# Performance work log

Measured on AMD Instinct MI355X. Metric: run time of the kernel, lower is better.

## Reference

```python
import jax, jax.numpy as jnp
import numpy as np

N_HEADS = 16
D_MODEL = 1024
D_HEAD = D_MODEL // N_HEADS  # 64


def setup_inputs() -> dict:
    key = jax.random.key(0)
    ks = jax.random.split(key, 7)
    B, S = 16, 1024
    x = jax.random.normal(ks[0], (B, S, D_MODEL), dtype=jnp.float32)
    # Per-head torch Linear params: weight [out, in] = [D_HEAD, D_HEAD], bias [D_HEAD].
    # Xavier-uniform scale for square weight: sqrt(6/(fan_in+fan_out)).
    lim = float(np.sqrt(6.0 / (D_HEAD + D_HEAD)))
    blim = float(1.0 / np.sqrt(D_HEAD))  # torch default bias init U(-1/sqrt(fan_in), ...)
    Wq = jax.random.uniform(ks[1], (N_HEADS, D_HEAD, D_HEAD), jnp.float32, -lim, lim)
    Wk = jax.random.uniform(ks[2], (N_HEADS, D_HEAD, D_HEAD), jnp.float32, -lim, lim)
    Wv = jax.random.uniform(ks[3], (N_HEADS, D_HEAD, D_HEAD), jnp.float32, -lim, lim)
    bq = jax.random.uniform(ks[4], (N_HEADS, D_HEAD), jnp.float32, -blim, blim)
    bk = jax.random.uniform(ks[5], (N_HEADS, D_HEAD), jnp.float32, -blim, blim)
    bv = jax.random.uniform(ks[6], (N_HEADS, D_HEAD), jnp.float32, -blim, blim)
    return {"sequences": x, "Wq": Wq, "Wk": Wk, "Wv": Wv, "bq": bq, "bk": bk, "bv": bv}


def reference(sequences, Wq, Wk, Wv, bq, bk, bv):
    B, S, D = sequences.shape
    H, dh = N_HEADS, D_HEAD
    # Split feature dim into heads: [B, S, H, dh] (same chunks the torch loop slices).
    x = sequences.reshape(B, S, H, dh)
    # torch Linear: y = x @ W.T + b  -> einsum over the 'in' axis of W[out, in].
    q = jnp.einsum("bshd,hed->bshe", x, Wq) + bq  # [B,S,H,dh]
    k = jnp.einsum("bshd,hed->bshe", x, Wk) + bk
    v = jnp.einsum("bshd,hed->bshe", x, Wv) + bv
    scale = 1.0 / jnp.sqrt(jnp.asarray(dh, dtype=sequences.dtype))
    scores = jnp.einsum("bshe,bthe->bhst", q, k) * scale  # [B,H,S,S]
    weights = jax.nn.softmax(scores, axis=-1)
    attended = jnp.einsum("bhst,bthe->bshe", weights, v)  # [B,S,H,dh]
    # hstack over heads == concat along feature dim.
    return attended.reshape(B, S, D)
```

## Files before the change

### kernel.cpp

```cpp
#include <hip/hip_runtime.h>

constexpr int B_ = 16, S_ = 1024, H_ = 16, DH_ = 64, DM_ = 1024;

typedef short bf16x8 __attribute__((ext_vector_type(8)));
typedef unsigned short us8 __attribute__((ext_vector_type(8)));
typedef unsigned short us4 __attribute__((ext_vector_type(4)));
typedef float f32x4 __attribute__((ext_vector_type(4)));
typedef float f32x16 __attribute__((ext_vector_type(16)));
typedef unsigned u32x4 __attribute__((ext_vector_type(4)));

__device__ __forceinline__ unsigned short f2b(float f) {
    unsigned u = __builtin_bit_cast(unsigned, f);
    u += 0x7FFFu + ((u >> 16) & 1u);
    return (unsigned short)(u >> 16);
}

__device__ __forceinline__ int swz(int r, int c) { return (r << 6) + (c ^ ((r & 7) << 3)); }

__device__ __forceinline__ unsigned cvtpk(float lo, float hi) {
    unsigned r;
    asm("v_cvt_pk_bf16_f32 %0, %1, %2" : "=v"(r) : "v"(lo), "v"(hi));
    return r;
}
__device__ __forceinline__ void permswap(unsigned& a, unsigned& b) {
    asm volatile("v_permlane32_swap_b32 %0, %1" : "+v"(a), "+v"(b));
}

__device__ __forceinline__ void gload16(const unsigned short* g, unsigned short* l) {
    __builtin_amdgcn_global_load_lds(
        (const __attribute__((address_space(1))) void*)g,
        (__attribute__((address_space(3))) void*)l, 16, 0, 0);
}

#define BAR_VM(N) do { \
    asm volatile("s_waitcnt vmcnt(" #N ") lgkmcnt(0)" ::: "memory"); \
    __builtin_amdgcn_sched_barrier(0); \
    __builtin_amdgcn_s_barrier(); \
    __builtin_amdgcn_sched_barrier(0); \
} while (0)

#define QSCALE 0.18033688011112042f

__global__ __launch_bounds__(256) void proj_kernel(
    const float* __restrict__ x,
    const float* __restrict__ wq, const float* __restrict__ wk, const float* __restrict__ wv,
    const float* __restrict__ bq, const float* __restrict__ bk, const float* __restrict__ bv,
    unsigned short* __restrict__ qo, unsigned short* __restrict__ ko,
    unsigned short* __restrict__ vto)
{
    __shared__ unsigned short xs[128 * 64];
    __shared__ unsigned short wls[3][64 * 64];

    const int tid = threadIdx.x;
    const int bid = blockIdx.x;
    const int chunk = bid & 7, bh = bid >> 3;
    const int b = bh >> 4, h = bh & 15;
    const int s0 = chunk * 128;
    const int lane = tid & 63, w = tid >> 6;
    const int lr = lane & 15, lg = lane >> 4;

    #pragma unroll
    for (int it = 0; it < 4; ++it) {
        int item = it * 256 + tid;
        int row = item >> 3, c = (item & 7) << 3;
        const float* src = x + (size_t)(b * S_ + s0 + row) * DM_ + h * DH_ + c;
        float4 f0 = *(const float4*)src;
        float4 f1 = *(const float4*)(src + 4);
        us8 v = { f2b(f0.x), f2b(f0.y), f2b(f0.z), f2b(f0.w),
                  f2b(f1.x), f2b(f1.y), f2b(f1.z), f2b(f1.w) };
        *(us8*)&xs[swz(row, c)] = v;
    }
    const float* wsrc[3] = { wq, wk, wv };
    #pragma unroll
    for (int mtx = 0; mtx < 3; ++mtx) {
        const float scl = (mtx == 0) ? QSCALE : 1.0f;
        #pragma unroll
        for (int it = 0; it < 2; ++it) {
            int item = it * 256 + tid;
            int row = item >> 3, c = (item & 7) << 3;
            const float* src = wsrc[mtx] + (size_t)h * 4096 + row * 64 + c;
            float4 f0 = *(const float4*)src;
            float4 f1 = *(const float4*)(src + 4);
            us8 v = { f2b(f0.x * scl), f2b(f0.y * scl), f2b(f0.z * scl), f2b(f0.w * scl),
                      f2b(f1.x * scl), f2b(f1.y * scl), f2b(f1.z * scl), f2b(f1.w * scl) };
            *(us8*)&wls[mtx][swz(row, c)] = v;
        }
    }
    __syncthreads();

    bf16x8 af[2][2];
    #pragma unroll
    for (int mt = 0; mt < 2; ++mt)
        #pragma unroll
        for (int k2 = 0; k2 < 2; ++k2)
            af[mt][k2] = *(const bf16x8*)&xs[swz(w * 32 + mt * 16 + lr, k2 * 32 + lg * 8)];

    const float* bias[3] = { bq, bk, bv };
    #pragma unroll
    for (int mtx = 0; mtx < 3; ++mtx) {
        const float bscl = (mtx == 0) ? QSCALE : 1.0f;
        #pragma unroll
        for (int mt = 0; mt < 2; ++mt) {
            #pragma unroll
            for (int n4 = 0; n4 < 4; ++n4) {
                f32x4 acc = { 0.f, 0.f, 0.f, 0.f };
                #pragma unroll
                for (int k2 = 0; k2 < 2; ++k2) {
                    bf16x8 bf_ = *(const bf16x8*)&wls[mtx][swz(n4 * 16 + lr, k2 * 32 + lg * 8)];
                    acc = __builtin_amdgcn_mfma_f32_16x16x32_bf16(af[mt][k2], bf_, acc, 0, 0, 0);
                }
                const int e = n4 * 16 + lr;
                const float bb = bias[mtx][h * DH_ + e] * bscl;
                const int srow0 = s0 + w * 32 + mt * 16 + lg * 4;
                if (mtx == 0) {
                    #pragma unroll
                    for (int r = 0; r < 4; ++r)
                        qo[(size_t)(bh * S_ + srow0 + r) * 64 + e] = f2b(acc[r] + bb);
                } else if (mtx == 1) {
                    #pragma unroll
                    for (int r = 0; r < 4; ++r)
                        ko[(size_t)(bh * S_ + srow0 + r) * 64 + e] = f2b(acc[r] + bb);
                } else {
                    us4 pk = { f2b(acc[0] + bb), f2b(acc[1] + bb),
                               f2b(acc[2] + bb), f2b(acc[3] + bb) };
                    *(us4*)&vto[(size_t)(bh * 64 + e) * S_ + srow0] = pk;
                }
            }
        }
    }
}

__device__ __forceinline__ void qk_tile(const unsigned short* K, const bf16x8 (&qf)[4],
                                        const f32x16& zro, f32x16& p0, f32x16& p1,
                                        int l31, int hi8)
{
    __builtin_amdgcn_s_setprio(1);
    {
        bf16x8 ka0 = *(const bf16x8*)&K[swz(l31,      hi8)];
        bf16x8 ka1 = *(const bf16x8*)&K[swz(32 + l31, hi8)];
        p0 = __builtin_amdgcn_mfma_f32_32x32x16_bf16(ka0, qf[0], zro, 0, 0, 0);
        p1 = __builtin_amdgcn_mfma_f32_32x32x16_bf16(ka1, qf[0], zro, 0, 0, 0);
    }
    #pragma unroll
    for (int s = 1; s < 4; ++s) {
        bf16x8 ka0 = *(const bf16x8*)&K[swz(l31,      s * 16 + hi8)];
        bf16x8 ka1 = *(const bf16x8*)&K[swz(32 + l31, s * 16 + hi8)];
        p0 = __builtin_amdgcn_mfma_f32_32x32x16_bf16(ka0, qf[s], p0, 0, 0, 0);
        p1 = __builtin_amdgcn_mfma_f32_32x32x16_bf16(ka1, qf[s], p1, 0, 0, 0);
    }
    __builtin_amdgcn_s_setprio(0);
}

__device__ __forceinline__ void pv_tile(f32x16& p0, f32x16& p1, const unsigned short* V,
                                        const bf16x8& ones, f32x16& o0, f32x16& o1,
                                        f32x16& lsum, int l31, int hi8)
{
    #pragma unroll
    for (int i = 0; i < 16; ++i) {
        p0[i] = __builtin_amdgcn_exp2f(p0[i]);
        p1[i] = __builtin_amdgcn_exp2f(p1[i]);
    }
    bf16x8 pa[4];
    {
        unsigned a0 = cvtpk(p0[0], p0[1]),  b0 = cvtpk(p0[4], p0[5]);
        unsigned a1 = cvtpk(p0[2], p0[3]),  b1 = cvtpk(p0[6], p0[7]);
        permswap(a0, b0); permswap(a1, b1);
        u32x4 t0 = { a0, a1, b0, b1 };
        pa[0] = __builtin_bit_cast(bf16x8, t0);
        unsigned a2 = cvtpk(p0[8], p0[9]),   b2 = cvtpk(p0[12], p0[13]);
        unsigned a3 = cvtpk(p0[10], p0[11]), b3 = cvtpk(p0[14], p0[15]);
        permswap(a2, b2); permswap(a3, b3);
        u32x4 t1 = { a2, a3, b2, b3 };
        pa[1] = __builtin_bit_cast(bf16x8, t1);
        unsigned a4 = cvtpk(p1[0], p1[1]),  b4 = cvtpk(p1[4], p1[5]);
        unsigned a5 = cvtpk(p1[2], p1[3]),  b5 = cvtpk(p1[6], p1[7]);
        permswap(a4, b4); permswap(a5, b5);
        u32x4 t2 = { a4, a5, b4, b5 };
        pa[2] = __builtin_bit_cast(bf16x8, t2);
        unsigned a6 = cvtpk(p1[8], p1[9]),   b6 = cvtpk(p1[12], p1[13]);
        unsigned a7 = cvtpk(p1[10], p1[11]), b7 = cvtpk(p1[14], p1[15]);
        permswap(a6, b6); permswap(a7, b7);
        u32x4 t3 = { a6, a7, b6, b7 };
        pa[3] = __builtin_bit_cast(bf16x8, t3);
    }
    __builtin_amdgcn_s_setprio(1);
    #pragma unroll
    for (int s = 0; s < 4; ++s) {
        bf16x8 vb0 = *(const bf16x8*)&V[swz(l31,      s * 16 + hi8)];
        bf16x8 vb1 = *(const bf16x8*)&V[swz(32 + l31, s * 16 + hi8)];
        o0 = __builtin_amdgcn_mfma_f32_32x32x16_bf16(pa[s], vb0, o0, 0, 0, 0);
        o1 = __builtin_amdgcn_mfma_f32_32x32x16_bf16(pa[s], vb1, o1, 0, 0, 0);
        lsum = __builtin_amdgcn_mfma_f32_32x32x16_bf16(pa[s], ones, lsum, 0, 0, 0);
    }
    __builtin_amdgcn_s_setprio(0);
}

__global__ __launch_bounds__(256) void attn_kernel(
    const unsigned short* __restrict__ qw, const unsigned short* __restrict__ kw,
    const unsigned short* __restrict__ vtw, float* __restrict__ out)
{
    __shared__ unsigned short ks[4][64 * 64];
    __shared__ unsigned short vs[4][64 * 64];

    const int tid = threadIdx.x, lane = tid & 63, w = tid >> 6;
    int bid = blockIdx.x;
    bid = (bid & 7) * 256 + (bid >> 3);
    const int qt = bid & 7, bh = bid >> 3;
    const int b = bh >> 4, h = bh & 15;
    const int q0 = qt * 128;
    const int l31 = lane & 31, hi = lane >> 5, hi8 = hi << 3;

    const unsigned short* kbase = kw + (size_t)bh * S_ * 64;
    const unsigned short* vbase = vtw + (size_t)bh * 64 * S_;

    const int srow8 = lane >> 3;
    const int colsw = ((lane & 7) ^ (lane >> 3)) << 3;

    auto stage = [&](int t) {
        const int bf = t & 3;
        const int n1 = t * 64;
        #pragma unroll
        for (int i = 0; i < 2; ++i) {
            const int br = i * 32 + (w << 3);
            gload16(kbase + (size_t)(n1 + br + srow8) * 64 + colsw, &ks[bf][br * 64]);
            gload16(vbase + (size_t)(br + srow8) * S_ + n1 + colsw, &vs[bf][br * 64]);
        }
    };

    bf16x8 qf[4];
    {
        const unsigned short* qp = qw + (size_t)(bh * S_ + q0 + w * 32 + l31) * 64 + hi8;
        #pragma unroll
        for (int s = 0; s < 4; ++s) qf[s] = *(const bf16x8*)(qp + s * 16);
    }

    const short ONE = (short)0x3F80;
    const bf16x8 ones = { ONE, ONE, ONE, ONE, ONE, ONE, ONE, ONE };

    f32x16 o0, o1, lsum, zro;
    #pragma unroll
    for (int i = 0; i < 16; ++i) { o0[i] = 0.f; o1[i] = 0.f; lsum[i] = 0.f; zro[i] = 0.f; }

    stage(0);
    stage(1);
    stage(2);
    BAR_VM(8);

    f32x16 pA0, pA1, pB0, pB1;
    qk_tile(&ks[0][0], qf, zro, pA0, pA1, l31, hi8);

    constexpr int NT = S_ / 64;
    #pragma unroll 1
    for (int tt = 0; tt < 7; ++tt) {
        const int t0 = 2 * tt;
        BAR_VM(4);
        stage(t0 + 3);
        qk_tile(&ks[(t0 + 1) & 3][0], qf, zro, pB0, pB1, l31, hi8);
        pv_tile(pA0, pA1, &vs[t0 & 3][0], ones, o0, o1, lsum, l31, hi8);
        BAR_VM(4);
        if (t0 + 4 < NT) stage(t0 + 4);
        qk_tile(&ks[(t0 + 2) & 3][0], qf, zro, pA0, pA1, l31, hi8);
        pv_tile(pB0, pB1, &vs[(t0 + 1) & 3][0], ones, o0, o1, lsum, l31, hi8);
    }
    BAR_VM(0);
    qk_tile(&ks[15 & 3][0], qf, zro, pB0, pB1, l31, hi8);
    pv_tile(pA0, pA1, &vs[14 & 3][0], ones, o0, o1, lsum, l31, hi8);
    pv_tile(pB0, pB1, &vs[15 & 3][0], ones, o0, o1, lsum, l31, hi8);

    #pragma unroll
    for (int r = 0; r < 16; ++r) {
        const int q = (r & 3) + 8 * (r >> 2) + (hi << 2);
        const float iv = 1.0f / lsum[r];
        float* op = out + (size_t)(b * S_ + q0 + w * 32 + q) * DM_ + h * DH_ + l31;
        op[0]  = o0[r] * iv;
        op[32] = o1[r] * iv;
    }
}

extern "C" void kernel_launch(void* const* d_in, const int* in_sizes, int n_in,
                              void* d_out, int out_size, void* d_ws, size_t ws_size,
                              hipStream_t stream) {
    const float* x  = (const float*)d_in[0];
    const float* wq = (const float*)d_in[1];
    const float* wk = (const float*)d_in[2];
    const float* wv = (const float*)d_in[3];
    const float* bq = (const float*)d_in[4];
    const float* bk = (const float*)d_in[5];
    const float* bv = (const float*)d_in[6];
    float* out = (float*)d_out;

    const size_t per = (size_t)B_ * H_ * S_ * DH_;
    unsigned short* qws  = (unsigned short*)d_ws;
    unsigned short* kws  = qws + per;
    unsigned short* vtws = kws + per;

    proj_kernel<<<dim3(2048), dim3(256), 0, stream>>>(x, wq, wk, wv, bq, bk, bv,
                                                      qws, kws, vtws);
    attn_kernel<<<dim3(2048), dim3(256), 0, stream>>>(qws, kws, vtws, out);
}
```

Measured before the change: 129.4 us.

## Process two 32-row query tiles per wave to reuse K/V LDS reads

Each wave now handles 64 query rows as two 32-row sub-tiles that share every K and V fragment loaded from LDS. This halves the block count and the total K/V traffic per query. The software-pipelined QK/PV interleave across tiles is replaced by a simple per-tile loop, so the overlap between the QK MFMAs of one tile and the exp/PV of the previous one is lost. Register pressure goes up, and with half as many blocks the GPU may be less well occupied.

```diff
diff --git a/kernel.cpp b/kernel.cpp
--- a/kernel.cpp
+++ b/kernel.cpp
@@ -130,69 +130,28 @@
     }
 }
 
-__device__ __forceinline__ void qk_tile(const unsigned short* K, const bf16x8 (&qf)[4],
-                                        const f32x16& zro, f32x16& p0, f32x16& p1,
-                                        int l31, int hi8)
+__device__ __forceinline__ void cvt_half(const f32x16& p0, const f32x16& p1, bf16x8 (&pa)[4])
 {
-    __builtin_amdgcn_s_setprio(1);
-    {
-        bf16x8 ka0 = *(const bf16x8*)&K[swz(l31,      hi8)];
-        bf16x8 ka1 = *(const bf16x8*)&K[swz(32 + l31, hi8)];
-        p0 = __builtin_amdgcn_mfma_f32_32x32x16_bf16(ka0, qf[0], zro, 0, 0, 0);
-        p1 = __builtin_amdgcn_mfma_f32_32x32x16_bf16(ka1, qf[0], zro, 0, 0, 0);
-    }
-    #pragma unroll
-    for (int s = 1; s < 4; ++s) {
-        bf16x8 ka0 = *(const bf16x8*)&K[swz(l31,      s * 16 + hi8)];
-        bf16x8 ka1 = *(const bf16x8*)&K[swz(32 + l31, s * 16 + hi8)];
-        p0 = __builtin_amdgcn_mfma_f32_32x32x16_bf16(ka0, qf[s], p0, 0, 0, 0);
-        p1 = __builtin_amdgcn_mfma_f32_32x32x16_bf16(ka1, qf[s], p1, 0, 0, 0);
-    }
-    __builtin_amdgcn_s_setprio(0);
-}
-
-__device__ __forceinline__ void pv_tile(f32x16& p0, f32x16& p1, const unsigned short* V,
-                                        const bf16x8& ones, f32x16& o0, f32x16& o1,
-                                        f32x16& lsum, int l31, int hi8)
-{
-    #pragma unroll
-    for (int i = 0; i < 16; ++i) {
-        p0[i] = __builtin_amdgcn_exp2f(p0[i]);
-        p1[i] = __builtin_amdgcn_exp2f(p1[i]);
-    }
-    bf16x8 pa[4];
-    {
-        unsigned a0 = cvtpk(p0[0], p0[1]),  b0 = cvtpk(p0[4], p0[5]);
-        unsigned a1 = cvtpk(p0[2], p0[3]),  b1 = cvtpk(p0[6], p0[7]);
-        permswap(a0, b0); permswap(a1, b1);
-        u32x4 t0 = { a0, a1, b0, b1 };
-        pa[0] = __builtin_bit_cast(bf16x8, t0);
-        unsigned a2 = cvtpk(p0[8], p0[9]),   b2 = cvtpk(p0[12], p0[13]);
-        unsigned a3 = cvtpk(p0[10], p0[11]), b3 = cvtpk(p0[14], p0[15]);
-        permswap(a2, b2); permswap(a3, b3);
-        u32x4 t1 = { a2, a3, b2, b3 };
-        pa[1] = __builtin_bit_cast(bf16x8, t1);
-        unsigned a4 = cvtpk(p1[0], p1[1]),  b4 = cvtpk(p1[4], p1[5]);
-        unsigned a5 = cvtpk(p1[2], p1[3]),  b5 = cvtpk(p1[6], p1[7]);
-        permswap(a4, b4); permswap(a5, b5);
-        u32x4 t2 = { a4, a5, b4, b5 };
-        pa[2] = __builtin_bit_cast(bf16x8, t2);
-        unsigned a6 = cvtpk(p1[8], p1[9]),   b6 = cvtpk(p1[12], p1[13]);
-        unsigned a7 = cvtpk(p1[10], p1[11]), b7 = cvtpk(p1[14], p1[15]);
-        permswap(a6, b6); permswap(a7, b7);
-        u32x4 t3 = { a6, a7, b6, b7 };
-        pa[3] = __builtin_bit_cast(bf16x8, t3);
-    }
-    __builtin_amdgcn_s_setprio(1);
-    #pragma unroll
-    for (int s = 0; s < 4; ++s) {
-        bf16x8 vb0 = *(const bf16x8*)&V[swz(l31,      s * 16 + hi8)];
-        bf16x8 vb1 = *(const bf16x8*)&V[swz(32 + l31, s * 16 + hi8)];
-        o0 = __builtin_amdgcn_mfma_f32_32x32x16_bf16(pa[s], vb0, o0, 0, 0, 0);
-        o1 = __builtin_amdgcn_mfma_f32_32x32x16_bf16(pa[s], vb1, o1, 0, 0, 0);
-        lsum = __builtin_amdgcn_mfma_f32_32x32x16_bf16(pa[s], ones, lsum, 0, 0, 0);
-    }
-    __builtin_amdgcn_s_setprio(0);
+    unsigned a0 = cvtpk(p0[0], p0[1]),  b0 = cvtpk(p0[4], p0[5]);
+    unsigned a1 = cvtpk(p0[2], p0[3]),  b1 = cvtpk(p0[6], p0[7]);
+    permswap(a0, b0); permswap(a1, b1);
+    u32x4 t0 = { a0, a1, b0, b1 };
+    pa[0] = __builtin_bit_cast(bf16x8, t0);
+    unsigned a2 = cvtpk(p0[8], p0[9]),   b2 = cvtpk(p0[12], p0[13]);
+    unsigned a3 = cvtpk(p0[10], p0[11]), b3 = cvtpk(p0[14], p0[15]);
+    permswap(a2, b2); permswap(a3, b3);
+    u32x4 t1 = { a2, a3, b2, b3 };
+    pa[1] = __builtin_bit_cast(bf16x8, t1);
+    unsigned a4 = cvtpk(p1[0], p1[1]),  b4 = cvtpk(p1[4], p1[5]);
+    unsigned a5 = cvtpk(p1[2], p1[3]),  b5 = cvtpk(p1[6], p1[7]);
+    permswap(a4, b4); permswap(a5, b5);
+    u32x4 t2 = { a4, a5, b4, b5 };
+    pa[2] = __builtin_bit_cast(bf16x8, t2);
+    unsigned a6 = cvtpk(p1[8], p1[9]),   b6 = cvtpk(p1[12], p1[13]);
+    unsigned a7 = cvtpk(p1[10], p1[11]), b7 = cvtpk(p1[14], p1[15]);
+    permswap(a6, b6); permswap(a7, b7);
+    u32x4 t3 = { a6, a7, b6, b7 };
+    pa[3] = __builtin_bit_cast(bf16x8, t3);
 }
 
 __global__ __launch_bounds__(256) void attn_kernel(
@@ -204,10 +163,10 @@
 
     const int tid = threadIdx.x, lane = tid & 63, w = tid >> 6;
     int bid = blockIdx.x;
-    bid = (bid & 7) * 256 + (bid >> 3);
-    const int qt = bid & 7, bh = bid >> 3;
+    bid = (bid & 7) * 128 + (bid >> 3);
+    const int qt = bid & 3, bh = bid >> 2;
     const int b = bh >> 4, h = bh & 15;
-    const int q0 = qt * 128;
+    const int q0w = qt * 256 + w * 64;
     const int l31 = lane & 31, hi = lane >> 5, hi8 = hi << 3;
 
     const unsigned short* kbase = kw + (size_t)bh * S_ * 64;
@@ -227,53 +186,102 @@
         }
     };
 
-    bf16x8 qf[4];
+    bf16x8 qfA[4], qfB[4];
     {
-        const unsigned short* qp = qw + (size_t)(bh * S_ + q0 + w * 32 + l31) * 64 + hi8;
-        #pragma unroll
-        for (int s = 0; s < 4; ++s) qf[s] = *(const bf16x8*)(qp + s * 16);
+        const unsigned short* qpA = qw + (size_t)(bh * S_ + q0w + l31) * 64 + hi8;
+        const unsigned short* qpB = qw + (size_t)(bh * S_ + q0w + 32 + l31) * 64 + hi8;
+        #pragma unroll
+        for (int s = 0; s < 4; ++s) {
+            qfA[s] = *(const bf16x8*)(qpA + s * 16);
+            qfB[s] = *(const bf16x8*)(qpB + s * 16);
+        }
     }
 
     const short ONE = (short)0x3F80;
     const bf16x8 ones = { ONE, ONE, ONE, ONE, ONE, ONE, ONE, ONE };
 
-    f32x16 o0, o1, lsum, zro;
-    #pragma unroll
-    for (int i = 0; i < 16; ++i) { o0[i] = 0.f; o1[i] = 0.f; lsum[i] = 0.f; zro[i] = 0.f; }
+    f32x16 oA0, oA1, oB0, oB1, lsumA, lsumB, zro;
+    #pragma unroll
+    for (int i = 0; i < 16; ++i) {
+        oA0[i] = 0.f; oA1[i] = 0.f; oB0[i] = 0.f; oB1[i] = 0.f;
+        lsumA[i] = 0.f; lsumB[i] = 0.f; zro[i] = 0.f;
+    }
 
     stage(0);
     stage(1);
     stage(2);
-    BAR_VM(8);
-
-    f32x16 pA0, pA1, pB0, pB1;
-    qk_tile(&ks[0][0], qf, zro, pA0, pA1, l31, hi8);
 
     constexpr int NT = S_ / 64;
     #pragma unroll 1
-    for (int tt = 0; tt < 7; ++tt) {
-        const int t0 = 2 * tt;
-        BAR_VM(4);
-        stage(t0 + 3);
-        qk_tile(&ks[(t0 + 1) & 3][0], qf, zro, pB0, pB1, l31, hi8);
-        pv_tile(pA0, pA1, &vs[t0 & 3][0], ones, o0, o1, lsum, l31, hi8);
-        BAR_VM(4);
-        if (t0 + 4 < NT) stage(t0 + 4);
-        qk_tile(&ks[(t0 + 2) & 3][0], qf, zro, pA0, pA1, l31, hi8);
-        pv_tile(pB0, pB1, &vs[(t0 + 1) & 3][0], ones, o0, o1, lsum, l31, hi8);
-    }
-    BAR_VM(0);
-    qk_tile(&ks[15 & 3][0], qf, zro, pB0, pB1, l31, hi8);
-    pv_tile(pA0, pA1, &vs[14 & 3][0], ones, o0, o1, lsum, l31, hi8);
-    pv_tile(pB0, pB1, &vs[15 & 3][0], ones, o0, o1, lsum, l31, hi8);
+    for (int t = 0; t < NT; ++t) {
+        if (t < 14)       { BAR_VM(8); }
+        else if (t == 14) { BAR_VM(4); }
+        else              { BAR_VM(0); }
+        if (t + 3 < NT) stage(t + 3);
+
+        const int buf = t & 3;
+        const unsigned short* K = &ks[buf][0];
+        const unsigned short* V = &vs[buf][0];
+
+        f32x16 pA0, pA1, pB0, pB1;
+        __builtin_amdgcn_s_setprio(1);
+        {
+            bf16x8 ka0 = *(const bf16x8*)&K[swz(l31,      hi8)];
+            bf16x8 ka1 = *(const bf16x8*)&K[swz(32 + l31, hi8)];
+            pA0 = __builtin_amdgcn_mfma_f32_32x32x16_bf16(ka0, qfA[0], zro, 0, 0, 0);
+            pA1 = __builtin_amdgcn_mfma_f32_32x32x16_bf16(ka1, qfA[0], zro, 0, 0, 0);
+            pB0 = __builtin_amdgcn_mfma_f32_32x32x16_bf16(ka0, qfB[0], zro, 0, 0, 0);
+            pB1 = __builtin_amdgcn_mfma_f32_32x32x16_bf16(ka1, qfB[0], zro, 0, 0, 0);
+        }
+        #pragma unroll
+        for (int s = 1; s < 4; ++s) {
+            bf16x8 ka0 = *(const bf16x8*)&K[swz(l31,      s * 16 + hi8)];
+            bf16x8 ka1 = *(const bf16x8*)&K[swz(32 + l31, s * 16 + hi8)];
+            pA0 = __builtin_amdgcn_mfma_f32_32x32x16_bf16(ka0, qfA[s], pA0, 0, 0, 0);
+            pA1 = __builtin_amdgcn_mfma_f32_32x32x16_bf16(ka1, qfA[s], pA1, 0, 0, 0);
+            pB0 = __builtin_amdgcn_mfma_f32_32x32x16_bf16(ka0, qfB[s], pB0, 0, 0, 0);
+            pB1 = __builtin_amdgcn_mfma_f32_32x32x16_bf16(ka1, qfB[s], pB1, 0, 0, 0);
+        }
+        __builtin_amdgcn_s_setprio(0);
+
+        #pragma unroll
+        for (int i = 0; i < 16; ++i) {
+            pA0[i] = __builtin_amdgcn_exp2f(pA0[i]);
+            pA1[i] = __builtin_amdgcn_exp2f(pA1[i]);
+            pB0[i] = __builtin_amdgcn_exp2f(pB0[i]);
+            pB1[i] = __builtin_amdgcn_exp2f(pB1[i]);
+        }
+
+        bf16x8 paA[4], paB[4];
+        cvt_half(pA0, pA1, paA);
+        cvt_half(pB0, pB1, paB);
+
+        __builtin_amdgcn_s_setprio(1);
+        #pragma unroll
+        for (int s = 0; s < 4; ++s) {
+            bf16x8 vb0 = *(const bf16x8*)&V[swz(l31,      s * 16 + hi8)];
+            bf16x8 vb1 = *(const bf16x8*)&V[swz(32 + l31, s * 16 + hi8)];
+            oA0 = __builtin_amdgcn_mfma_f32_32x32x16_bf16(paA[s], vb0, oA0, 0, 0, 0);
+            oA1 = __builtin_amdgcn_mfma_f32_32x32x16_bf16(paA[s], vb1, oA1, 0, 0, 0);
+            oB0 = __builtin_amdgcn_mfma_f32_32x32x16_bf16(paB[s], vb0, oB0, 0, 0, 0);
+            oB1 = __builtin_amdgcn_mfma_f32_32x32x16_bf16(paB[s], vb1, oB1, 0, 0, 0);
+            lsumA = __builtin_amdgcn_mfma_f32_32x32x16_bf16(paA[s], ones, lsumA, 0, 0, 0);
+            lsumB = __builtin_amdgcn_mfma_f32_32x32x16_bf16(paB[s], ones, lsumB, 0, 0, 0);
+        }
+        __builtin_amdgcn_s_setprio(0);
+    }
 
     #pragma unroll
     for (int r = 0; r < 16; ++r) {
         const int q = (r & 3) + 8 * (r >> 2) + (hi << 2);
-        const float iv = 1.0f / lsum[r];
-        float* op = out + (size_t)(b * S_ + q0 + w * 32 + q) * DM_ + h * DH_ + l31;
-        op[0]  = o0[r] * iv;
-        op[32] = o1[r] * iv;
+        const float ivA = 1.0f / lsumA[r];
+        const float ivB = 1.0f / lsumB[r];
+        float* opA = out + (size_t)(b * S_ + q0w + q) * DM_ + h * DH_ + l31;
+        float* opB = out + (size_t)(b * S_ + q0w + 32 + q) * DM_ + h * DH_ + l31;
+        opA[0]  = oA0[r] * ivA;
+        opA[32] = oA1[r] * ivA;
+        opB[0]  = oB0[r] * ivB;
+        opB[32] = oB1[r] * ivB;
     }
 }
 
@@ -296,5 +304,5 @@
 
     proj_kernel<<<dim3(2048), dim3(256), 0, stream>>>(x, wq, wk, wv, bq, bk, bv,
                                                       qws, kws, vtws);
-    attn_kernel<<<dim3(2048), dim3(256), 0, stream>>>(qws, kws, vtws, out);
-}
+    attn_kernel<<<dim3(1024), dim3(256), 0, stream>>>(qws, kws, vtws, out);
+}
```

Measured after the change: 167.9 us. +29.7%, slower.

## Drop ones-MFMA row sum, use triple buffering and target three blocks per CU

Applied to the files above, without the earlier changes.

Removes the software-pipelined two-tile QK/PV interleave and replaces it with a simple per-tile loop over a 3-deep LDS ring buffer instead of 4-deep. The row sum previously computed by an extra MFMA against a ones vector is now a VALU reduction plus a cross-half shuffle, and the normalizer is broadcast with a shuffle at the end. Launch bounds request 3 blocks per CU, cutting register and LDS use to raise occupancy. The cost is losing the explicit overlap of QK MFMAs with exp/convert work and adding VALU adds to each tile.

```diff
diff --git a/kernel.cpp b/kernel.cpp
--- a/kernel.cpp
+++ b/kernel.cpp
@@ -130,77 +130,12 @@
     }
 }
 
-__device__ __forceinline__ void qk_tile(const unsigned short* K, const bf16x8 (&qf)[4],
-                                        const f32x16& zro, f32x16& p0, f32x16& p1,
-                                        int l31, int hi8)
-{
-    __builtin_amdgcn_s_setprio(1);
-    {
-        bf16x8 ka0 = *(const bf16x8*)&K[swz(l31,      hi8)];
-        bf16x8 ka1 = *(const bf16x8*)&K[swz(32 + l31, hi8)];
-        p0 = __builtin_amdgcn_mfma_f32_32x32x16_bf16(ka0, qf[0], zro, 0, 0, 0);
-        p1 = __builtin_amdgcn_mfma_f32_32x32x16_bf16(ka1, qf[0], zro, 0, 0, 0);
-    }
-    #pragma unroll
-    for (int s = 1; s < 4; ++s) {
-        bf16x8 ka0 = *(const bf16x8*)&K[swz(l31,      s * 16 + hi8)];
-        bf16x8 ka1 = *(const bf16x8*)&K[swz(32 + l31, s * 16 + hi8)];
-        p0 = __builtin_amdgcn_mfma_f32_32x32x16_bf16(ka0, qf[s], p0, 0, 0, 0);
-        p1 = __builtin_amdgcn_mfma_f32_32x32x16_bf16(ka1, qf[s], p1, 0, 0, 0);
-    }
-    __builtin_amdgcn_s_setprio(0);
-}
-
-__device__ __forceinline__ void pv_tile(f32x16& p0, f32x16& p1, const unsigned short* V,
-                                        const bf16x8& ones, f32x16& o0, f32x16& o1,
-                                        f32x16& lsum, int l31, int hi8)
-{
-    #pragma unroll
-    for (int i = 0; i < 16; ++i) {
-        p0[i] = __builtin_amdgcn_exp2f(p0[i]);
-        p1[i] = __builtin_amdgcn_exp2f(p1[i]);
-    }
-    bf16x8 pa[4];
-    {
-        unsigned a0 = cvtpk(p0[0], p0[1]),  b0 = cvtpk(p0[4], p0[5]);
-        unsigned a1 = cvtpk(p0[2], p0[3]),  b1 = cvtpk(p0[6], p0[7]);
-        permswap(a0, b0); permswap(a1, b1);
-        u32x4 t0 = { a0, a1, b0, b1 };
-        pa[0] = __builtin_bit_cast(bf16x8, t0);
-        unsigned a2 = cvtpk(p0[8], p0[9]),   b2 = cvtpk(p0[12], p0[13]);
-        unsigned a3 = cvtpk(p0[10], p0[11]), b3 = cvtpk(p0[14], p0[15]);
-        permswap(a2, b2); permswap(a3, b3);
-        u32x4 t1 = { a2, a3, b2, b3 };
-        pa[1] = __builtin_bit_cast(bf16x8, t1);
-        unsigned a4 = cvtpk(p1[0], p1[1]),  b4 = cvtpk(p1[4], p1[5]);
-        unsigned a5 = cvtpk(p1[2], p1[3]),  b5 = cvtpk(p1[6], p1[7]);
-        permswap(a4, b4); permswap(a5, b5);
-        u32x4 t2 = { a4, a5, b4, b5 };
-        pa[2] = __builtin_bit_cast(bf16x8, t2);
-        unsigned a6 = cvtpk(p1[8], p1[9]),   b6 = cvtpk(p1[12], p1[13]);
-        unsigned a7 = cvtpk(p1[10], p1[11]), b7 = cvtpk(p1[14], p1[15]);
-        permswap(a6, b6); permswap(a7, b7);
-        u32x4 t3 = { a6, a7, b6, b7 };
-        pa[3] = __builtin_bit_cast(bf16x8, t3);
-    }
-    __builtin_amdgcn_s_setprio(1);
-    #pragma unroll
-    for (int s = 0; s < 4; ++s) {
-        bf16x8 vb0 = *(const bf16x8*)&V[swz(l31,      s * 16 + hi8)];
-        bf16x8 vb1 = *(const bf16x8*)&V[swz(32 + l31, s * 16 + hi8)];
-        o0 = __builtin_amdgcn_mfma_f32_32x32x16_bf16(pa[s], vb0, o0, 0, 0, 0);
-        o1 = __builtin_amdgcn_mfma_f32_32x32x16_bf16(pa[s], vb1, o1, 0, 0, 0);
-        lsum = __builtin_amdgcn_mfma_f32_32x32x16_bf16(pa[s], ones, lsum, 0, 0, 0);
-    }
-    __builtin_amdgcn_s_setprio(0);
-}
-
-__global__ __launch_bounds__(256) void attn_kernel(
+__global__ __launch_bounds__(256, 3) void attn_kernel(
     const unsigned short* __restrict__ qw, const unsigned short* __restrict__ kw,
     const unsigned short* __restrict__ vtw, float* __restrict__ out)
 {
-    __shared__ unsigned short ks[4][64 * 64];
-    __shared__ unsigned short vs[4][64 * 64];
+    __shared__ unsigned short ks[3][64 * 64];
+    __shared__ unsigned short vs[3][64 * 64];
 
     const int tid = threadIdx.x, lane = tid & 63, w = tid >> 6;
     int bid = blockIdx.x;
@@ -217,7 +152,7 @@
     const int colsw = ((lane & 7) ^ (lane >> 3)) << 3;
 
     auto stage = [&](int t) {
-        const int bf = t & 3;
+        const int bf = t % 3;
         const int n1 = t * 64;
         #pragma unroll
         for (int i = 0; i < 2; ++i) {
@@ -234,43 +169,95 @@
         for (int s = 0; s < 4; ++s) qf[s] = *(const bf16x8*)(qp + s * 16);
     }
 
-    const short ONE = (short)0x3F80;
-    const bf16x8 ones = { ONE, ONE, ONE, ONE, ONE, ONE, ONE, ONE };
-
-    f32x16 o0, o1, lsum, zro;
-    #pragma unroll
-    for (int i = 0; i < 16; ++i) { o0[i] = 0.f; o1[i] = 0.f; lsum[i] = 0.f; zro[i] = 0.f; }
+    f32x16 o0, o1, zro;
+    #pragma unroll
+    for (int i = 0; i < 16; ++i) { o0[i] = 0.f; o1[i] = 0.f; zro[i] = 0.f; }
+    float lreg = 0.f;
 
     stage(0);
     stage(1);
-    stage(2);
-    BAR_VM(8);
-
-    f32x16 pA0, pA1, pB0, pB1;
-    qk_tile(&ks[0][0], qf, zro, pA0, pA1, l31, hi8);
 
     constexpr int NT = S_ / 64;
     #pragma unroll 1
-    for (int tt = 0; tt < 7; ++tt) {
-        const int t0 = 2 * tt;
-        BAR_VM(4);
-        stage(t0 + 3);
-        qk_tile(&ks[(t0 + 1) & 3][0], qf, zro, pB0, pB1, l31, hi8);
-        pv_tile(pA0, pA1, &vs[t0 & 3][0], ones, o0, o1, lsum, l31, hi8);
-        BAR_VM(4);
-        if (t0 + 4 < NT) stage(t0 + 4);
-        qk_tile(&ks[(t0 + 2) & 3][0], qf, zro, pA0, pA1, l31, hi8);
-        pv_tile(pB0, pB1, &vs[(t0 + 1) & 3][0], ones, o0, o1, lsum, l31, hi8);
-    }
-    BAR_VM(0);
-    qk_tile(&ks[15 & 3][0], qf, zro, pB0, pB1, l31, hi8);
-    pv_tile(pA0, pA1, &vs[14 & 3][0], ones, o0, o1, lsum, l31, hi8);
-    pv_tile(pB0, pB1, &vs[15 & 3][0], ones, o0, o1, lsum, l31, hi8);
-
+    for (int t = 0; t < NT; ++t) {
+        if (t < NT - 1) { BAR_VM(4); }
+        else            { BAR_VM(0); }
+        if (t + 2 < NT) stage(t + 2);
+
+        const int buf = t % 3;
+        const unsigned short* K = &ks[buf][0];
+        const unsigned short* V = &vs[buf][0];
+
+        f32x16 p0, p1;
+        __builtin_amdgcn_s_setprio(1);
+        {
+            bf16x8 ka0 = *(const bf16x8*)&K[swz(l31,      hi8)];
+            bf16x8 ka1 = *(const bf16x8*)&K[swz(32 + l31, hi8)];
+            p0 = __builtin_amdgcn_mfma_f32_32x32x16_bf16(ka0, qf[0], zro, 0, 0, 0);
+            p1 = __builtin_amdgcn_mfma_f32_32x32x16_bf16(ka1, qf[0], zro, 0, 0, 0);
+        }
+        #pragma unroll
+        for (int s = 1; s < 4; ++s) {
+            bf16x8 ka0 = *(const bf16x8*)&K[swz(l31,      s * 16 + hi8)];
+            bf16x8 ka1 = *(const bf16x8*)&K[swz(32 + l31, s * 16 + hi8)];
+            p0 = __builtin_amdgcn_mfma_f32_32x32x16_bf16(ka0, qf[s], p0, 0, 0, 0);
+            p1 = __builtin_amdgcn_mfma_f32_32x32x16_bf16(ka1, qf[s], p1, 0, 0, 0);
+        }
+        __builtin_amdgcn_s_setprio(0);
+
+        #pragma unroll
+        for (int i = 0; i < 16; ++i) {
+            p0[i] = __builtin_amdgcn_exp2f(p0[i]);
+            p1[i] = __builtin_amdgcn_exp2f(p1[i]);
+        }
+        {
+            float rs = 0.f;
+            #pragma unroll
+            for (int i = 0; i < 16; ++i) rs += p0[i] + p1[i];
+            rs += __shfl_xor(rs, 32);
+            lreg += rs;
+        }
+
+        bf16x8 pa[4];
+        {
+            unsigned a0 = cvtpk(p0[0], p0[1]),  b0 = cvtpk(p0[4], p0[5]);
+            unsigned a1 = cvtpk(p0[2], p0[3]),  b1 = cvtpk(p0[6], p0[7]);
+            permswap(a0, b0); permswap(a1, b1);
+            u32x4 t0 = { a0, a1, b0, b1 };
+            pa[0] = __builtin_bit_cast(bf16x8, t0);
+            unsigned a2 = cvtpk(p0[8], p0[9]),   b2 = cvtpk(p0[12], p0[13]);
+            unsigned a3 = cvtpk(p0[10], p0[11]), b3 = cvtpk(p0[14], p0[15]);
+            permswap(a2, b2); permswap(a3, b3);
+            u32x4 t1 = { a2, a3, b2, b3 };
+            pa[1] = __builtin_bit_cast(bf16x8, t1);
+            unsigned a4 = cvtpk(p1[0], p1[1]),  b4 = cvtpk(p1[4], p1[5]);
+            unsigned a5 = cvtpk(p1[2], p1[3]),  b5 = cvtpk(p1[6], p1[7]);
+            permswap(a4, b4); permswap(a5, b5);
+            u32x4 t2 = { a4, a5, b4, b5 };
+            pa[2] = __builtin_bit_cast(bf16x8, t2);
+            unsigned a6 = cvtpk(p1[8], p1[9]),   b6 = cvtpk(p1[12], p1[13]);
+            unsigned a7 = cvtpk(p1[10], p1[11]), b7 = cvtpk(p1[14], p1[15]);
+            permswap(a6, b6); permswap(a7, b7);
+            u32x4 t3 = { a6, a7, b6, b7 };
+            pa[3] = __builtin_bit_cast(bf16x8, t3);
+        }
+
+        __builtin_amdgcn_s_setprio(1);
+        #pragma unroll
+        for (int s = 0; s < 4; ++s) {
+            bf16x8 vb0 = *(const bf16x8*)&V[swz(l31,      s * 16 + hi8)];
+            bf16x8 vb1 = *(const bf16x8*)&V[swz(32 + l31, s * 16 + hi8)];
+            o0 = __builtin_amdgcn_mfma_f32_32x32x16_bf16(pa[s], vb0, o0, 0, 0, 0);
+            o1 = __builtin_amdgcn_mfma_f32_32x32x16_bf16(pa[s], vb1, o1, 0, 0, 0);
+        }
+        __builtin_amdgcn_s_setprio(0);
+    }
+
+    const float linv = 1.0f / lreg;
     #pragma unroll
     for (int r = 0; r < 16; ++r) {
         const int q = (r & 3) + 8 * (r >> 2) + (hi << 2);
-        const float iv = 1.0f / lsum[r];
+        const float iv = __shfl(linv, q);
         float* op = out + (size_t)(b * S_ + q0 + w * 32 + q) * DM_ + h * DH_ + l31;
         op[0]  = o0[r] * iv;
         op[32] = o1[r] * iv;
```

After: 120.9 us. 1.07x faster.
